# Performance work log

Hardware: AMD Instinct MI355X
Metric: run time of the kernel (lower is better)

Reference implementation:

```python
import jax, jax.numpy as jnp
import numpy as np

def setup_inputs() -> dict:
    key = jax.random.key(0)
    k1, k2 = jax.random.split(key)
    B, C = 65536, 1000
    outputs = jax.random.normal(k1, (B, C), dtype=jnp.float32)
    labels = jax.random.randint(k2, (B,), 0, C, dtype=jnp.int64)
    return {"outputs": outputs, "labels": labels}

def reference(outputs, labels):
    B = outputs.shape[0]
    # ground-truth score per row: [B, 1]
    ground = jnp.take_along_axis(outputs, labels[:, None].astype(jnp.int32), axis=1)
    # hinge margin per class: max(0, y_j - y_true + 1); j == label contributes exactly 1
    margins = jnp.maximum(outputs - ground + 1.0, 0.0)
    per_row = jnp.sum(margins, axis=1) - 1.0  # remove the j == label term
    loss = jnp.sum(per_row) / B
    correct_count = jnp.sum(jnp.argmax(outputs, axis=1) == labels)
    return (loss, correct_count)
```

## Files before the change

### kernel.cpp

```cpp
#include <hip/hip_runtime.h>
#include <math.h>


#define BLOCK 256
#define GRID1 2048
#define WPB   (BLOCK / 64)
#define NWAVE (GRID1 * WPB)

__global__ __launch_bounds__(BLOCK) void msrp_partial(
    const float* __restrict__ outp, const int* __restrict__ labels,
    float* __restrict__ partS, int* __restrict__ partC, int B, int C) {
  const int lane    = threadIdx.x & 63;
  const int wib     = threadIdx.x >> 6;
  const int wave_id = blockIdx.x * WPB + wib;
  const int R       = B / NWAVE;
  const int r0      = wave_id * R;

  int   mylab = 0;
  float myg   = 0.0f;
  if (lane < R && r0 + lane < B) {
    mylab = labels[r0 + lane];
    myg   = outp[(size_t)(r0 + lane) * C + mylab];
  }

  float s = 0.0f;
  int correct = 0;
  const int C4 = C >> 2;

  for (int k = 0; k < R; ++k) {
    const int row = r0 + k;
    if (row >= B) break;
    const int   label = __shfl(mylab, k, 64);
    const float g     = __shfl(myg, k, 64);
    const float base  = 1.0f - g;
    const float4* rp4 = (const float4*)(outp + (size_t)row * C);

    bool viol = false;
    for (int j = lane; j < C4; j += 64) {
      float4 v = rp4[j];
      s += fmaxf(v.x + base, 0.0f) + fmaxf(v.y + base, 0.0f) +
           fmaxf(v.z + base, 0.0f) + fmaxf(v.w + base, 0.0f);
      const int j4 = j << 2;
      viol |= (v.x > g) | ((v.x == g) & (j4     < label));
      viol |= (v.y > g) | ((v.y == g) & (j4 + 1 < label));
      viol |= (v.z > g) | ((v.z == g) & (j4 + 2 < label));
      viol |= (v.w > g) | ((v.w == g) & (j4 + 3 < label));
    }
    const float* rowp = (const float*)rp4;
    for (int j = (C4 << 2) + lane; j < C; j += 64) {
      float v = rowp[j];
      s += fmaxf(v + base, 0.0f);
      viol |= (v > g) | ((v == g) & (j < label));
    }

    unsigned long long m = __ballot(viol);
    if (lane == 0) correct += (m == 0ULL) ? 1 : 0;
  }

  for (int off = 32; off > 0; off >>= 1) s += __shfl_down(s, off, 64);

  __shared__ float ls[WPB];
  __shared__ int   cs[WPB];
  if (lane == 0) { ls[wib] = s; cs[wib] = correct; }
  __syncthreads();
  if (threadIdx.x == 0) {
    float S = 0.0f; int cc = 0;
    for (int w = 0; w < WPB; ++w) { S += ls[w]; cc += cs[w]; }
    partS[blockIdx.x] = S;
    partC[blockIdx.x] = cc;
  }
}

__global__ __launch_bounds__(BLOCK) void msrp_finalize(
    const float* __restrict__ partS, const int* __restrict__ partC,
    float* __restrict__ dst, int B, int nPart) {
  const int tid = threadIdx.x;
  float s = 0.0f; int c = 0;
  for (int i = tid; i < nPart; i += BLOCK) { s += partS[i]; c += partC[i]; }

  const int lane = tid & 63;
  const int wib  = tid >> 6;
  for (int off = 32; off > 0; off >>= 1) {
    s += __shfl_down(s, off, 64);
    c += __shfl_down(c, off, 64);
  }
  __shared__ float ls[WPB];
  __shared__ int   cs[WPB];
  if (lane == 0) { ls[wib] = s; cs[wib] = c; }
  __syncthreads();
  if (tid == 0) {
    float S = 0.0f; int cc = 0;
    for (int w = 0; w < WPB; ++w) { S += ls[w]; cc += cs[w]; }
    dst[0] = S / (float)B - 1.0f;
    dst[1] = (float)cc;
  }
}

extern "C" void kernel_launch(void* const* d_in, const int* in_sizes, int n_in,
                              void* d_out, int out_size, void* d_ws, size_t ws_size,
                              hipStream_t stream) {
  const float* outp   = (const float*)d_in[0];
  const int*   labels = (const int*)d_in[1];
  float*       dst    = (float*)d_out;

  const int B = in_sizes[1];
  const int C = in_sizes[0] / B;

  float* partS = (float*)d_ws;
  int*   partC = (int*)(partS + GRID1);

  msrp_partial<<<GRID1, BLOCK, 0, stream>>>(outp, labels, partS, partC, B, C);
  msrp_finalize<<<1, BLOCK, 0, stream>>>(partS, partC, dst, B, GRID1);
}
```

Measured before the change: 358.9 us.

## Fuse finalize into partial kernel via last-block atomic and unroll C=1000 row loads

Merges the two-kernel reduction into one kernel: each block publishes its partials, takes a ticket from an atomic counter, and the last block performs the final reduction. Adds a C==1000 specialised path that issues all four float4 loads per row up front, and splits the accumulator into four independent sums to raise memory-level parallelism. Also generalises the row split with ceil division and a fallback for large R. Costs an extra memset launch and atomic/fence overhead.

```diff
diff --git a/kernel.cpp b/kernel.cpp
--- a/kernel.cpp
+++ b/kernel.cpp
@@ -7,92 +7,130 @@
 #define WPB   (BLOCK / 64)
 #define NWAVE (GRID1 * WPB)
 
-__global__ __launch_bounds__(BLOCK) void msrp_partial(
+__global__ __launch_bounds__(BLOCK) void msrp_fused(
     const float* __restrict__ outp, const int* __restrict__ labels,
-    float* __restrict__ partS, int* __restrict__ partC, int B, int C) {
+    float* __restrict__ partS, int* __restrict__ partC,
+    unsigned int* __restrict__ counter, float* __restrict__ dst,
+    int B, int C) {
   const int lane    = threadIdx.x & 63;
   const int wib     = threadIdx.x >> 6;
   const int wave_id = blockIdx.x * WPB + wib;
-  const int R       = B / NWAVE;
+  const int R       = (B + NWAVE - 1) / NWAVE;
   const int r0      = wave_id * R;
 
   int   mylab = 0;
   float myg   = 0.0f;
-  if (lane < R && r0 + lane < B) {
+  if (lane < R && lane < 64 && r0 + lane < B) {
     mylab = labels[r0 + lane];
     myg   = outp[(size_t)(r0 + lane) * C + mylab];
   }
 
-  float s = 0.0f;
+  float s0 = 0.f, s1 = 0.f, s2 = 0.f, s3 = 0.f;
   int correct = 0;
-  const int C4 = C >> 2;
 
-  for (int k = 0; k < R; ++k) {
-    const int row = r0 + k;
-    if (row >= B) break;
-    const int   label = __shfl(mylab, k, 64);
-    const float g     = __shfl(myg, k, 64);
-    const float base  = 1.0f - g;
-    const float4* rp4 = (const float4*)(outp + (size_t)row * C);
+#define CONSUME(v, jb)                                                   \
+  do {                                                                   \
+    s0 += fmaxf((v).x + base, 0.0f);                                     \
+    s1 += fmaxf((v).y + base, 0.0f);                                     \
+    s2 += fmaxf((v).z + base, 0.0f);                                     \
+    s3 += fmaxf((v).w + base, 0.0f);                                     \
+    viol |= ((v).x > g) | (((v).x == g) & ((jb)     < label));           \
+    viol |= ((v).y > g) | (((v).y == g) & ((jb) + 1 < label));           \
+    viol |= ((v).z > g) | (((v).z == g) & ((jb) + 2 < label));           \
+    viol |= ((v).w > g) | (((v).w == g) & ((jb) + 3 < label));           \
+  } while (0)
 
-    bool viol = false;
-    for (int j = lane; j < C4; j += 64) {
-      float4 v = rp4[j];
-      s += fmaxf(v.x + base, 0.0f) + fmaxf(v.y + base, 0.0f) +
-           fmaxf(v.z + base, 0.0f) + fmaxf(v.w + base, 0.0f);
-      const int j4 = j << 2;
-      viol |= (v.x > g) | ((v.x == g) & (j4     < label));
-      viol |= (v.y > g) | ((v.y == g) & (j4 + 1 < label));
-      viol |= (v.z > g) | ((v.z == g) & (j4 + 2 < label));
-      viol |= (v.w > g) | ((v.w == g) & (j4 + 3 < label));
+  if (C == 1000) {
+    for (int k = 0; k < R; ++k) {
+      const int row = r0 + k;
+      if (row >= B) break;
+      const int   label = (R <= 64) ? __shfl(mylab, k, 64) : labels[row];
+      const float g     = (R <= 64) ? __shfl(myg, k, 64)
+                                    : outp[(size_t)row * C + label];
+      const float base  = 1.0f - g;
+      const float4* rp4 = (const float4*)(outp + (size_t)row * 1000);
+
+      float4 v0 = rp4[lane];
+      float4 v1 = rp4[lane + 64];
+      float4 v2 = rp4[lane + 128];
+      const bool h3 = (lane < 58);
+      float4 v3;
+      if (h3) v3 = rp4[lane + 192];
+
+      bool viol = false;
+      CONSUME(v0, lane * 4);
+      CONSUME(v1, (lane + 64) * 4);
+      CONSUME(v2, (lane + 128) * 4);
+      if (h3) CONSUME(v3, (lane + 192) * 4);
+
+      const unsigned long long m = __ballot(viol);
+      if (lane == 0) correct += (m == 0ULL) ? 1 : 0;
     }
-    const float* rowp = (const float*)rp4;
-    for (int j = (C4 << 2) + lane; j < C; j += 64) {
-      float v = rowp[j];
-      s += fmaxf(v + base, 0.0f);
-      viol |= (v > g) | ((v == g) & (j < label));
+  } else {
+    const int C4 = C >> 2;
+    for (int k = 0; k < R; ++k) {
+      const int row = r0 + k;
+      if (row >= B) break;
+      const int   label = (R <= 64) ? __shfl(mylab, k, 64) : labels[row];
+      const float g     = (R <= 64) ? __shfl(myg, k, 64)
+                                    : outp[(size_t)row * C + label];
+      const float base  = 1.0f - g;
+      const float4* rp4 = (const float4*)(outp + (size_t)row * C);
+      bool viol = false;
+      for (int j = lane; j < C4; j += 64) {
+        float4 v = rp4[j];
+        CONSUME(v, j << 2);
+      }
+      const float* rowp = (const float*)rp4;
+      for (int j = (C4 << 2) + lane; j < C; j += 64) {
+        float v = rowp[j];
+        s0 += fmaxf(v + base, 0.0f);
+        viol |= (v > g) | ((v == g) & (j < label));
+      }
+      const unsigned long long m = __ballot(viol);
+      if (lane == 0) correct += (m == 0ULL) ? 1 : 0;
     }
+  }
+#undef CONSUME
 
-    unsigned long long m = __ballot(viol);
-    if (lane == 0) correct += (m == 0ULL) ? 1 : 0;
-  }
-
+  float s = (s0 + s1) + (s2 + s3);
   for (int off = 32; off > 0; off >>= 1) s += __shfl_down(s, off, 64);
 
   __shared__ float ls[WPB];
   __shared__ int   cs[WPB];
+  __shared__ bool  amLast;
   if (lane == 0) { ls[wib] = s; cs[wib] = correct; }
   __syncthreads();
   if (threadIdx.x == 0) {
-    float S = 0.0f; int cc = 0;
+    float S = 0.f; int cc = 0;
     for (int w = 0; w < WPB; ++w) { S += ls[w]; cc += cs[w]; }
     partS[blockIdx.x] = S;
     partC[blockIdx.x] = cc;
+    __threadfence();
+    const unsigned int old = atomicAdd(counter, 1u);
+    amLast = (old == (unsigned)GRID1 - 1u);
   }
-}
+  __syncthreads();
 
-__global__ __launch_bounds__(BLOCK) void msrp_finalize(
-    const float* __restrict__ partS, const int* __restrict__ partC,
-    float* __restrict__ dst, int B, int nPart) {
-  const int tid = threadIdx.x;
-  float s = 0.0f; int c = 0;
-  for (int i = tid; i < nPart; i += BLOCK) { s += partS[i]; c += partC[i]; }
-
-  const int lane = tid & 63;
-  const int wib  = tid >> 6;
-  for (int off = 32; off > 0; off >>= 1) {
-    s += __shfl_down(s, off, 64);
-    c += __shfl_down(c, off, 64);
-  }
-  __shared__ float ls[WPB];
-  __shared__ int   cs[WPB];
-  if (lane == 0) { ls[wib] = s; cs[wib] = c; }
-  __syncthreads();
-  if (tid == 0) {
-    float S = 0.0f; int cc = 0;
-    for (int w = 0; w < WPB; ++w) { S += ls[w]; cc += cs[w]; }
-    dst[0] = S / (float)B - 1.0f;
-    dst[1] = (float)cc;
+  if (amLast) {
+    __threadfence();
+    float fs = 0.f; int fc = 0;
+    for (int i = threadIdx.x; i < GRID1; i += BLOCK) {
+      fs += partS[i];
+      fc += partC[i];
+    }
+    for (int off = 32; off > 0; off >>= 1) {
+      fs += __shfl_down(fs, off, 64);
+      fc += __shfl_down(fc, off, 64);
+    }
+    if (lane == 0) { ls[wib] = fs; cs[wib] = fc; }
+    __syncthreads();
+    if (threadIdx.x == 0) {
+      float S = 0.f; int cc = 0;
+      for (int w = 0; w < WPB; ++w) { S += ls[w]; cc += cs[w]; }
+      dst[0] = S / (float)B - 1.0f;
+      dst[1] = (float)cc;
+    }
   }
 }
 
@@ -106,9 +144,12 @@
   const int B = in_sizes[1];
   const int C = in_sizes[0] / B;
 
-  float* partS = (float*)d_ws;
-  int*   partC = (int*)(partS + GRID1);
+  float*        partS   = (float*)d_ws;
+  int*          partC   = (int*)(partS + GRID1);
+  unsigned int* counter = (unsigned int*)(partC + GRID1);
 
-  msrp_partial<<<GRID1, BLOCK, 0, stream>>>(outp, labels, partS, partC, B, C);
-  msrp_finalize<<<1, BLOCK, 0, stream>>>(partS, partC, dst, B, GRID1);
+  hipMemsetAsync(counter, 0, sizeof(unsigned int), stream);
+
+  msrp_fused<<<GRID1, BLOCK, 0, stream>>>(outp, labels, partS, partC,
+                                          counter, dst, B, C);
 }
```

Result: slower. 454.9 us (+26.8%).

## Specialize C=1000 path with fully unrolled loads and next-row prefetch

Applied to the files above, without the earlier changes.

Adds a fast path for C == 1000 in which each lane loads its four float4 chunks of a row directly, with the inner loop unrolled, and issues the loads for the next row before computing on the current one (software double buffering). The sum is split across four independent accumulators to shorten the dependency chain, and launch bounds request 8 waves per SIMD. The aim is to keep more memory requests in flight on this bandwidth-bound reduction. In exchange the kernel uses more registers, and the float summation order changes slightly.

```diff
diff --git a/kernel.cpp b/kernel.cpp
--- a/kernel.cpp
+++ b/kernel.cpp
@@ -7,56 +7,94 @@
 #define WPB   (BLOCK / 64)
 #define NWAVE (GRID1 * WPB)
 
-__global__ __launch_bounds__(BLOCK) void msrp_partial(
+#define CONSUME(v, jb)                                                   \
+  do {                                                                   \
+    s0 += fmaxf((v).x + base, 0.0f);                                     \
+    s1 += fmaxf((v).y + base, 0.0f);                                     \
+    s2 += fmaxf((v).z + base, 0.0f);                                     \
+    s3 += fmaxf((v).w + base, 0.0f);                                     \
+    viol |= ((v).x > g) | (((v).x == g) & ((jb)     < label));           \
+    viol |= ((v).y > g) | (((v).y == g) & ((jb) + 1 < label));           \
+    viol |= ((v).z > g) | (((v).z == g) & ((jb) + 2 < label));           \
+    viol |= ((v).w > g) | (((v).w == g) & ((jb) + 3 < label));           \
+  } while (0)
+
+__global__ __launch_bounds__(BLOCK, 8) void msrp_partial(
     const float* __restrict__ outp, const int* __restrict__ labels,
     float* __restrict__ partS, int* __restrict__ partC, int B, int C) {
   const int lane    = threadIdx.x & 63;
   const int wib     = threadIdx.x >> 6;
   const int wave_id = blockIdx.x * WPB + wib;
-  const int R       = B / NWAVE;
+  const int R       = (B + NWAVE - 1) / NWAVE;
   const int r0      = wave_id * R;
 
   int   mylab = 0;
   float myg   = 0.0f;
-  if (lane < R && r0 + lane < B) {
+  if (lane < R && lane < 64 && r0 + lane < B) {
     mylab = labels[r0 + lane];
     myg   = outp[(size_t)(r0 + lane) * C + mylab];
   }
 
-  float s = 0.0f;
+  float s0 = 0.f, s1 = 0.f, s2 = 0.f, s3 = 0.f;
   int correct = 0;
-  const int C4 = C >> 2;
 
-  for (int k = 0; k < R; ++k) {
-    const int row = r0 + k;
-    if (row >= B) break;
-    const int   label = __shfl(mylab, k, 64);
-    const float g     = __shfl(myg, k, 64);
-    const float base  = 1.0f - g;
-    const float4* rp4 = (const float4*)(outp + (size_t)row * C);
+  if (C == 1000 && r0 + R <= B) {
+    const int idx3 = (lane < 58) ? lane + 192 : 249;
+    const bool h3  = (lane < 58);
+    const float* rowbase = outp + (size_t)r0 * 1000;
 
-    bool viol = false;
-    for (int j = lane; j < C4; j += 64) {
-      float4 v = rp4[j];
-      s += fmaxf(v.x + base, 0.0f) + fmaxf(v.y + base, 0.0f) +
-           fmaxf(v.z + base, 0.0f) + fmaxf(v.w + base, 0.0f);
-      const int j4 = j << 2;
-      viol |= (v.x > g) | ((v.x == g) & (j4     < label));
-      viol |= (v.y > g) | ((v.y == g) & (j4 + 1 < label));
-      viol |= (v.z > g) | ((v.z == g) & (j4 + 2 < label));
-      viol |= (v.w > g) | ((v.w == g) & (j4 + 3 < label));
+    const float4* rp = (const float4*)rowbase;
+    float4 a0 = rp[lane], a1 = rp[lane + 64], a2 = rp[lane + 128], a3 = rp[idx3];
+
+    for (int k = 0; k < R; ++k) {
+      float4 b0, b1, b2, b3;
+      if (k + 1 < R) {
+        const float4* rn = (const float4*)(rowbase + (size_t)(k + 1) * 1000);
+        b0 = rn[lane]; b1 = rn[lane + 64]; b2 = rn[lane + 128]; b3 = rn[idx3];
+      } else {
+        b0 = a0; b1 = a1; b2 = a2; b3 = a3;
+      }
+
+      const int   label = __shfl(mylab, k, 64);
+      const float g     = __shfl(myg, k, 64);
+      const float base  = 1.0f - g;
+      bool viol = false;
+      CONSUME(a0, lane * 4);
+      CONSUME(a1, (lane + 64) * 4);
+      CONSUME(a2, (lane + 128) * 4);
+      if (h3) CONSUME(a3, (lane + 192) * 4);
+
+      const unsigned long long m = __ballot(viol);
+      if (lane == 0) correct += (m == 0ULL) ? 1 : 0;
+
+      a0 = b0; a1 = b1; a2 = b2; a3 = b3;
     }
-    const float* rowp = (const float*)rp4;
-    for (int j = (C4 << 2) + lane; j < C; j += 64) {
-      float v = rowp[j];
-      s += fmaxf(v + base, 0.0f);
-      viol |= (v > g) | ((v == g) & (j < label));
+  } else {
+    const int C4 = C >> 2;
+    for (int k = 0; k < R; ++k) {
+      const int row = r0 + k;
+      if (row >= B) break;
+      const int   label = __shfl(mylab, k, 64);
+      const float g     = __shfl(myg, k, 64);
+      const float base  = 1.0f - g;
+      const float4* rp4 = (const float4*)(outp + (size_t)row * C);
+      bool viol = false;
+      for (int j = lane; j < C4; j += 64) {
+        float4 v = rp4[j];
+        CONSUME(v, j << 2);
+      }
+      const float* rowp = (const float*)rp4;
+      for (int j = (C4 << 2) + lane; j < C; j += 64) {
+        float v = rowp[j];
+        s0 += fmaxf(v + base, 0.0f);
+        viol |= (v > g) | ((v == g) & (j < label));
+      }
+      const unsigned long long m = __ballot(viol);
+      if (lane == 0) correct += (m == 0ULL) ? 1 : 0;
     }
-
-    unsigned long long m = __ballot(viol);
-    if (lane == 0) correct += (m == 0ULL) ? 1 : 0;
   }
 
+  float s = (s0 + s1) + (s2 + s3);
   for (int off = 32; off > 0; off >>= 1) s += __shfl_down(s, off, 64);
 
   __shared__ float ls[WPB];
@@ -64,7 +102,7 @@
   if (lane == 0) { ls[wib] = s; cs[wib] = correct; }
   __syncthreads();
   if (threadIdx.x == 0) {
-    float S = 0.0f; int cc = 0;
+    float S = 0.f; int cc = 0;
     for (int w = 0; w < WPB; ++w) { S += ls[w]; cc += cs[w]; }
     partS[blockIdx.x] = S;
     partC[blockIdx.x] = cc;
@@ -89,7 +127,7 @@
   if (lane == 0) { ls[wib] = s; cs[wib] = c; }
   __syncthreads();
   if (tid == 0) {
-    float S = 0.0f; int cc = 0;
+    float S = 0.f; int cc = 0;
     for (int w = 0; w < WPB; ++w) { S += ls[w]; cc += cs[w]; }
     dst[0] = S / (float)B - 1.0f;
     dst[1] = (float)cc;
```

After: 356.6 us. Within noise of the previous version (-0.6%).
